# Kernel tuning notes

Hardware: AMD Instinct MI355X
Metric: run time of the kernel (lower is better)

Reference implementation:

```python
import math
import jax, jax.numpy as jnp
import numpy as np

SCALE = 64.0
MARGIN = 0.5
T = 0.2
COS_M = math.cos(MARGIN)
SIN_M = math.sin(MARGIN)
TH = math.cos(math.pi - MARGIN)
MM = math.sin(math.pi - MARGIN) * MARGIN
EPS = 1e-07

B, D, C = 512, 512, 100000


def setup_inputs() -> dict:
    key = jax.random.key(0)
    k1, k2, k3 = jax.random.split(key, 3)
    embedding = jax.random.normal(k1, (B, D), dtype=jnp.float32)
    # xavier_uniform for (num_classes, embed_size)
    limit = math.sqrt(6.0 / (C + D))
    weight = jax.random.uniform(k2, (C, D), dtype=jnp.float32, minval=-limit, maxval=limit)
    ground_truth = jax.random.randint(k3, (B,), 0, C, dtype=jnp.int64)
    return {"embedding": embedding, "weight": weight, "ground_truth": ground_truth}


def reference(embedding, weight, ground_truth):
    gt = ground_truth.astype(jnp.int32)
    e = embedding / jnp.linalg.norm(embedding, axis=1, keepdims=True)
    w = weight / jnp.linalg.norm(weight, axis=1, keepdims=True)
    # (B, C) cosine similarities
    cos_theta = jnp.clip(jnp.einsum('bd,cd->bc', e, w), -1.0 + EPS, 1.0 - EPS)
    pos = jnp.take_along_axis(cos_theta, gt[:, None], axis=1)  # (B, 1)
    sin_theta = jnp.sqrt(jnp.clip(1.0 - pos * pos, EPS, 1.0 - EPS))
    phi = pos * COS_M - sin_theta * SIN_M
    phi = jnp.where(pos > TH, phi, pos - MM)  # easy_margin=False branch
    # hard-example reweighting: fixed=False -> (t+1)*cos + t where cos > phi
    mask = cos_theta > phi  # phi broadcasts (B,1) -> (B,C)
    cos_theta = jnp.where(mask, (T + 1.0) * cos_theta + T, cos_theta)
    # scatter phi into the ground-truth column
    output = cos_theta.at[jnp.arange(B), gt].set(phi[:, 0])
    output = output * SCALE
    # mean cross-entropy
    logp = jax.nn.log_softmax(output, axis=1)
    loss = -jnp.mean(jnp.take_along_axis(logp, gt[:, None], axis=1))
    return loss
```

## Files before the change

### kernel.cpp

```cpp
#include <hip/hip_runtime.h>
#include <hip/hip_bf16.h>
#include <stdint.h>

typedef unsigned short u16;
typedef __attribute__((ext_vector_type(8))) short short8;
typedef __attribute__((ext_vector_type(4))) float floatx4;

#define B_   512
#define D_   512
#define C_   100000

#define SCALE_  64.0f
#define COSM_   0.8775825618903728f
#define SINM_   0.479425538604203f
#define TH_     (-0.8775825618903728f)
#define MM_     0.2397127693021015f
#define EPS_    1e-7f
#define SHIFT_  89.6f

#define BM 256
#define BN 64
#define BK 32

__device__ inline float wave_reduce_sum(float v) {
    v += __shfl_xor(v, 1);
    v += __shfl_xor(v, 2);
    v += __shfl_xor(v, 4);
    v += __shfl_xor(v, 8);
    v += __shfl_xor(v, 16);
    v += __shfl_xor(v, 32);
    return v;
}

__device__ inline u16 f2bf(float x) {
    union { float f; uint32_t u; } v; v.f = x;
    uint32_t r = v.u + 0x7fffu + ((v.u >> 16) & 1u);
    return (u16)(r >> 16);
}

__global__ __launch_bounds__(256) void norm_e_phi_kernel(
    const float* __restrict__ emb, const float* __restrict__ w_raw,
    const int* __restrict__ gt, u16* __restrict__ e_bf16,
    float* __restrict__ phi, float* __restrict__ rowsum) {
    if (threadIdx.x < 4) rowsum[blockIdx.x * 4 + threadIdx.x] = 0.0f;
    int wv = threadIdx.x >> 6;
    int lane = threadIdx.x & 63;
    int b = blockIdx.x * 4 + wv;
    const float4* rp = (const float4*)(emb + (long)b * D_);
    float4 f0 = rp[lane], f1 = rp[lane + 64];
    float sq = f0.x*f0.x + f0.y*f0.y + f0.z*f0.z + f0.w*f0.w
             + f1.x*f1.x + f1.y*f1.y + f1.z*f1.z + f1.w*f1.w;
    sq = wave_reduce_sum(sq);
    float rn = 1.0f / sqrtf(sq);
    f0.x *= rn; f0.y *= rn; f0.z *= rn; f0.w *= rn;
    f1.x *= rn; f1.y *= rn; f1.z *= rn; f1.w *= rn;
    uint2 p0, p1;
    p0.x = (uint32_t)f2bf(f0.x) | ((uint32_t)f2bf(f0.y) << 16);
    p0.y = (uint32_t)f2bf(f0.z) | ((uint32_t)f2bf(f0.w) << 16);
    p1.x = (uint32_t)f2bf(f1.x) | ((uint32_t)f2bf(f1.y) << 16);
    p1.y = (uint32_t)f2bf(f1.z) | ((uint32_t)f2bf(f1.w) << 16);
    uint2* ob = (uint2*)(e_bf16 + (long)b * D_);
    ob[lane] = p0;
    ob[lane + 64] = p1;

    int g = gt[b];
    const float4* wp = (const float4*)(w_raw + (long)g * D_);
    float4 w0 = wp[lane], w1 = wp[lane + 64];
    float dt = f0.x*w0.x + f0.y*w0.y + f0.z*w0.z + f0.w*w0.w
             + f1.x*w1.x + f1.y*w1.y + f1.z*w1.z + f1.w*w1.w;
    float wsq = w0.x*w0.x + w0.y*w0.y + w0.z*w0.z + w0.w*w0.w
              + w1.x*w1.x + w1.y*w1.y + w1.z*w1.z + w1.w*w1.w;
    dt = wave_reduce_sum(dt);
    wsq = wave_reduce_sum(wsq);
    if (lane == 0) {
        float pos = dt / sqrtf(wsq);
        pos = fminf(fmaxf(pos, -1.0f + EPS_), 1.0f - EPS_);
        float s2 = 1.0f - pos * pos;
        s2 = fminf(fmaxf(s2, EPS_), 1.0f - EPS_);
        float sin_t = sqrtf(s2);
        float ph = pos * COSM_ - sin_t * SINM_;
        ph = (pos > TH_) ? ph : (pos - MM_);
        phi[b] = ph;
    }
}

__device__ inline void cvt_store(const float4& v0, const float4& v1,
                                 u16* dst, float& sq) {
    union { u16 h[8]; uint4 q; } u;
    u.h[0] = f2bf(v0.x); u.h[1] = f2bf(v0.y);
    u.h[2] = f2bf(v0.z); u.h[3] = f2bf(v0.w);
    u.h[4] = f2bf(v1.x); u.h[5] = f2bf(v1.y);
    u.h[6] = f2bf(v1.z); u.h[7] = f2bf(v1.w);
    *(uint4*)dst = u.q;
    sq += v0.x*v0.x + v0.y*v0.y + v0.z*v0.z + v0.w*v0.w
        + v1.x*v1.x + v1.y*v1.y + v1.z*v1.z + v1.w*v1.w;
}

__global__ __launch_bounds__(256, 3) void gemm_arcface_fused(
    const u16* __restrict__ a_g,
    const float* __restrict__ w_g,
    const float* __restrict__ phi, const int* __restrict__ gt,
    float* __restrict__ rowsum) {
    __shared__ __align__(16) u16 b_tile[2][BN * BK];
    __shared__ float phi_s[BM];
    __shared__ int gt_s[BM];
    __shared__ float rnorm_s[BN];

    int tid = threadIdx.x;
    int c0 = (blockIdx.x >> 1) * BN;
    int m0 = (blockIdx.x & 1) * BM;

    phi_s[tid] = phi[m0 + tid];
    gt_s[tid] = gt[m0 + tid];

    int rb = tid >> 2;
    int bslot = tid & 3;
    int bkq = bslot ^ ((rb >> 1) & 3);
    long brow_g = min(c0 + rb, C_ - 1);
    const float4* b_src = (const float4*)(w_g + brow_g * (long)D_ + bkq * 8);
    u16* b_dst0 = &b_tile[0][rb * BK + bslot * 8];
    u16* b_dst1 = &b_tile[1][rb * BK + bslot * 8];

    int wv = tid >> 6, lane = tid & 63;
    int low4 = lane & 15, quad = lane >> 4;
    int lslot = quad ^ ((low4 >> 1) & 3);
    const u16* a_base = a_g + (long)(m0 + wv * 64 + low4) * D_ + quad * 8;
    int bf_off = low4 * BK + lslot * 8;

    floatx4 acc[4][4] = {};
    float sq = 0.0f;
    float4 bv[2][2];
    short8 afc[4];

    bv[0][0] = b_src[0]; bv[0][1] = b_src[1];
    cvt_store(bv[0][0], bv[0][1], b_dst0, sq);
    bv[1][0] = b_src[8]; bv[1][1] = b_src[9];
    __syncthreads();

#pragma unroll
    for (int kt = 0; kt < 16; kt++) {
        int p = kt & 1;
        if (kt < 14) {
            bv[p][0] = b_src[(kt + 2) * 8];
            bv[p][1] = b_src[(kt + 2) * 8 + 1];
        }
#pragma unroll
        for (int mi = 0; mi < 4; mi++)
            afc[mi] = *(const short8*)(a_base + (long)mi * 16 * D_ + kt * BK);
        short8 bf[4];
#pragma unroll
        for (int ni = 0; ni < 4; ni++)
            bf[ni] = *(const short8*)(&b_tile[p][ni * 16 * BK + bf_off]);
#pragma unroll
        for (int mi = 0; mi < 4; mi++)
#pragma unroll
            for (int ni = 0; ni < 4; ni++)
                acc[mi][ni] = __builtin_amdgcn_mfma_f32_16x16x32_bf16(
                    afc[mi], bf[ni], acc[mi][ni], 0, 0, 0);
        if (kt < 15)
            cvt_store(bv[1 - p][0], bv[1 - p][1], p ? b_dst0 : b_dst1, sq);
        __syncthreads();
    }

    sq += __shfl_xor(sq, 1);
    sq += __shfl_xor(sq, 2);
    if ((tid & 3) == 0) rnorm_s[rb] = 1.0f / sqrtf(sq);
    __syncthreads();

#pragma unroll
    for (int mi = 0; mi < 4; mi++) {
#pragma unroll
        for (int r = 0; r < 4; r++) {
            int rl = wv * 64 + mi * 16 + quad * 4 + r;
            float ph = phi_s[rl];
            int g = gt_s[rl];
            float s = 0.0f;
#pragma unroll
            for (int ni = 0; ni < 4; ni++) {
                int cl = ni * 16 + low4;
                int c = c0 + cl;
                float v = acc[mi][ni][r] * rnorm_s[cl];
                v = fminf(fmaxf(v, -1.0f + EPS_), 1.0f - EPS_);
                float logit = (v > ph) ? (1.2f * v + 0.2f) : v;
                logit *= SCALE_;
                if (c == g) logit = SCALE_ * ph;
                s += (c < C_) ? __expf(logit - SHIFT_) : 0.0f;
            }
            s += __shfl_xor(s, 1);
            s += __shfl_xor(s, 2);
            s += __shfl_xor(s, 4);
            s += __shfl_xor(s, 8);
            if (low4 == 0) atomicAdd(&rowsum[m0 + rl], s);
        }
    }
}

__global__ __launch_bounds__(256) void loss_kernel(
    const float* __restrict__ rowsum, const float* __restrict__ phi,
    float* __restrict__ out) {
    __shared__ float red[4];
    int tid = threadIdx.x;
    float s = 0.0f;
    for (int b = tid; b < B_; b += 256)
        s += logf(rowsum[b]) + SHIFT_ - SCALE_ * phi[b];
    s = wave_reduce_sum(s);
    int wv = tid >> 6, lane = tid & 63;
    if (lane == 0) red[wv] = s;
    __syncthreads();
    if (tid == 0) out[0] = (red[0] + red[1] + red[2] + red[3]) * (1.0f / B_);
}

extern "C" void kernel_launch(void* const* d_in, const int* in_sizes, int n_in,
                              void* d_out, int out_size, void* d_ws, size_t ws_size,
                              hipStream_t stream) {
    const float* emb = (const float*)d_in[0];
    const float* wgt = (const float*)d_in[1];
    const int* gt = (const int*)d_in[2];
    float* out = (float*)d_out;

    char* ws = (char*)d_ws;
    u16* e_bf16 = (u16*)(ws);
    float* phi = (float*)(ws + 524288);
    float* rowsum = (float*)(ws + 526336);

    norm_e_phi_kernel<<<B_ / 4, 256, 0, stream>>>(emb, wgt, gt, e_bf16, phi, rowsum);
    int nc = (C_ + BN - 1) / BN;
    gemm_arcface_fused<<<nc * 2, 256, 0, stream>>>(e_bf16, wgt, phi, gt, rowsum);
    loss_kernel<<<1, 256, 0, stream>>>(rowsum, phi, out);
}
```

Before: 449.1 us.

## Load weight fragments directly into registers, drop LDS staging and barriers

The GEMM no longer stages the fp32 weight tile through shared memory. Each wave loads its own B fragments straight from global memory into registers, converts them to bf16 with the packed intrinsic, and computes per-column norms with cross-lane shuffles. This removes the LDS writes and reads and the per-k-step __syncthreads. In exchange, each of the 4 waves redundantly loads the same weight rows, which quadruples global/L2 traffic for B, and the extra prefetch registers may lower occupancy.

Measured after the change: 683.6 us. +52.2%, slower.

```diff
diff --git a/kernel.cpp b/kernel.cpp
--- a/kernel.cpp
+++ b/kernel.cpp
@@ -20,7 +20,6 @@
 
 #define BM 256
 #define BN 64
-#define BK 32
 
 __device__ inline float wave_reduce_sum(float v) {
     v += __shfl_xor(v, 1);
@@ -84,16 +83,15 @@
     }
 }
 
-__device__ inline void cvt_store(const float4& v0, const float4& v1,
-                                 u16* dst, float& sq) {
-    union { u16 h[8]; uint4 q; } u;
-    u.h[0] = f2bf(v0.x); u.h[1] = f2bf(v0.y);
-    u.h[2] = f2bf(v0.z); u.h[3] = f2bf(v0.w);
-    u.h[4] = f2bf(v1.x); u.h[5] = f2bf(v1.y);
-    u.h[6] = f2bf(v1.z); u.h[7] = f2bf(v1.w);
-    *(uint4*)dst = u.q;
+__device__ inline short8 cvt_pack8(const float4 v0, const float4 v1, float& sq) {
+    union { __hip_bfloat162 b2[4]; short8 s; } u;
+    u.b2[0] = __float22bfloat162_rn(float2{v0.x, v0.y});
+    u.b2[1] = __float22bfloat162_rn(float2{v0.z, v0.w});
+    u.b2[2] = __float22bfloat162_rn(float2{v1.x, v1.y});
+    u.b2[3] = __float22bfloat162_rn(float2{v1.z, v1.w});
     sq += v0.x*v0.x + v0.y*v0.y + v0.z*v0.z + v0.w*v0.w
         + v1.x*v1.x + v1.y*v1.y + v1.z*v1.z + v1.w*v1.w;
+    return u.s;
 }
 
 __global__ __launch_bounds__(256, 3) void gemm_arcface_fused(
@@ -101,71 +99,79 @@
     const float* __restrict__ w_g,
     const float* __restrict__ phi, const int* __restrict__ gt,
     float* __restrict__ rowsum) {
-    __shared__ __align__(16) u16 b_tile[2][BN * BK];
     __shared__ float phi_s[BM];
     __shared__ int gt_s[BM];
-    __shared__ float rnorm_s[BN];
 
     int tid = threadIdx.x;
     int c0 = (blockIdx.x >> 1) * BN;
     int m0 = (blockIdx.x & 1) * BM;
-
     phi_s[tid] = phi[m0 + tid];
     gt_s[tid] = gt[m0 + tid];
-
-    int rb = tid >> 2;
-    int bslot = tid & 3;
-    int bkq = bslot ^ ((rb >> 1) & 3);
-    long brow_g = min(c0 + rb, C_ - 1);
-    const float4* b_src = (const float4*)(w_g + brow_g * (long)D_ + bkq * 8);
-    u16* b_dst0 = &b_tile[0][rb * BK + bslot * 8];
-    u16* b_dst1 = &b_tile[1][rb * BK + bslot * 8];
+    __syncthreads();
 
     int wv = tid >> 6, lane = tid & 63;
     int low4 = lane & 15, quad = lane >> 4;
-    int lslot = quad ^ ((low4 >> 1) & 3);
-    const u16* a_base = a_g + (long)(m0 + wv * 64 + low4) * D_ + quad * 8;
-    int bf_off = low4 * BK + lslot * 8;
+
+    const float4* bp[4];
+#pragma unroll
+    for (int ni = 0; ni < 4; ni++) {
+        long brow = min(c0 + ni * 16 + low4, C_ - 1);
+        bp[ni] = (const float4*)(w_g + brow * (long)D_) + quad * 2;
+    }
+    const u16* a_row = a_g + (long)(m0 + wv * 64 + low4) * D_ + quad * 8;
 
     floatx4 acc[4][4] = {};
-    float sq = 0.0f;
-    float4 bv[2][2];
-    short8 afc[4];
-
-    bv[0][0] = b_src[0]; bv[0][1] = b_src[1];
-    cvt_store(bv[0][0], bv[0][1], b_dst0, sq);
-    bv[1][0] = b_src[8]; bv[1][1] = b_src[9];
-    __syncthreads();
+    float sq4[4] = {0.0f, 0.0f, 0.0f, 0.0f};
+
+    float4 bnx[4][2];
+    short8 anx[4];
+#pragma unroll
+    for (int ni = 0; ni < 4; ni++) {
+        bnx[ni][0] = bp[ni][0];
+        bnx[ni][1] = bp[ni][1];
+    }
+#pragma unroll
+    for (int mi = 0; mi < 4; mi++)
+        anx[mi] = *(const short8*)(a_row + (long)mi * 16 * D_);
 
 #pragma unroll
     for (int kt = 0; kt < 16; kt++) {
-        int p = kt & 1;
-        if (kt < 14) {
-            bv[p][0] = b_src[(kt + 2) * 8];
-            bv[p][1] = b_src[(kt + 2) * 8 + 1];
+        float4 bt[4][2];
+        short8 at[4];
+#pragma unroll
+        for (int ni = 0; ni < 4; ni++) { bt[ni][0] = bnx[ni][0]; bt[ni][1] = bnx[ni][1]; }
+#pragma unroll
+        for (int mi = 0; mi < 4; mi++) at[mi] = anx[mi];
+        if (kt < 15) {
+#pragma unroll
+            for (int ni = 0; ni < 4; ni++) {
+                bnx[ni][0] = bp[ni][(kt + 1) * 8];
+                bnx[ni][1] = bp[ni][(kt + 1) * 8 + 1];
+            }
+#pragma unroll
+            for (int mi = 0; mi < 4; mi++)
+                anx[mi] = *(const short8*)(a_row + (long)mi * 16 * D_ + (kt + 1) * 32);
         }
-#pragma unroll
-        for (int mi = 0; mi < 4; mi++)
-            afc[mi] = *(const short8*)(a_base + (long)mi * 16 * D_ + kt * BK);
-        short8 bf[4];
+        short8 bfr[4];
 #pragma unroll
         for (int ni = 0; ni < 4; ni++)
-            bf[ni] = *(const short8*)(&b_tile[p][ni * 16 * BK + bf_off]);
+            bfr[ni] = cvt_pack8(bt[ni][0], bt[ni][1], sq4[ni]);
 #pragma unroll
         for (int mi = 0; mi < 4; mi++)
 #pragma unroll
             for (int ni = 0; ni < 4; ni++)
                 acc[mi][ni] = __builtin_amdgcn_mfma_f32_16x16x32_bf16(
-                    afc[mi], bf[ni], acc[mi][ni], 0, 0, 0);
-        if (kt < 15)
-            cvt_store(bv[1 - p][0], bv[1 - p][1], p ? b_dst0 : b_dst1, sq);
-        __syncthreads();
-    }
-
-    sq += __shfl_xor(sq, 1);
-    sq += __shfl_xor(sq, 2);
-    if ((tid & 3) == 0) rnorm_s[rb] = 1.0f / sqrtf(sq);
-    __syncthreads();
+                    at[mi], bfr[ni], acc[mi][ni], 0, 0, 0);
+    }
+
+    float rnorm[4];
+#pragma unroll
+    for (int ni = 0; ni < 4; ni++) {
+        float s = sq4[ni];
+        s += __shfl_xor(s, 16);
+        s += __shfl_xor(s, 32);
+        rnorm[ni] = 1.0f / sqrtf(s);
+    }
 
 #pragma unroll
     for (int mi = 0; mi < 4; mi++) {
@@ -177,9 +183,8 @@
             float s = 0.0f;
 #pragma unroll
             for (int ni = 0; ni < 4; ni++) {
-                int cl = ni * 16 + low4;
-                int c = c0 + cl;
-                float v = acc[mi][ni][r] * rnorm_s[cl];
+                int c = c0 + ni * 16 + low4;
+                float v = acc[mi][ni][r] * rnorm[ni];
                 v = fminf(fmaxf(v, -1.0f + EPS_), 1.0f - EPS_);
                 float logit = (v > ph) ? (1.2f * v + 0.2f) : v;
                 logit *= SCALE_;
```
